# Kernel tuning notes

Hardware: AMD Instinct MI355X
Metric: run time of the kernel (lower is better)

Reference implementation:

```python
import jax, jax.numpy as jnp
import numpy as np


def setup_inputs() -> dict:
    key = jax.random.key(0)
    kq, kk, kv = jax.random.split(key, 3)
    B, T, D = 32, 2048, 64
    return {
        "queries": jax.random.normal(kq, (B, T, D), dtype=jnp.float32),
        "keys": jax.random.normal(kk, (B, T, D), dtype=jnp.float32),
        "values": jax.random.normal(kv, (B, T, D), dtype=jnp.float32),
    }


def reference(queries, keys, values):
    # scores: [B, T, T] = Q K^T / sqrt(d)
    d = queries.shape[-1]
    scale = 1.0 / jnp.sqrt(jnp.asarray(d, dtype=queries.dtype))
    scores = jnp.einsum("btd,bsd->bts", queries, keys) * scale
    T = scores.shape[-1]
    # causal lower-triangular mask; masked positions -> -inf before softmax
    causal = jnp.tril(jnp.ones((T, T), dtype=bool))
    scores = jnp.where(causal[None, :, :], scores, -jnp.inf)
    attn = jax.nn.softmax(scores, axis=-1)
    # eval mode: no dropout
    return jnp.einsum("bts,bsd->btd", attn, values)
```

## Files before the change

### kernel.cpp

```cpp
#include <hip/hip_runtime.h>
#include <hip/hip_bf16.h>

typedef __bf16 bf16;
typedef bf16 bf16x2 __attribute__((ext_vector_type(2)));
typedef bf16 bf16x8 __attribute__((ext_vector_type(8)));
typedef float f32x2 __attribute__((ext_vector_type(2)));
typedef float f32x4 __attribute__((ext_vector_type(4)));
typedef float f32x16 __attribute__((ext_vector_type(16)));
typedef unsigned int uint;

namespace {
constexpr int kB  = 32;
constexpr int kT  = 2048;
constexpr int kD  = 64;
constexpr int QB  = 128;
constexpr int KVB = 64;
constexpr float THR = 8.f;
}

__global__ __launch_bounds__(256, 2)
void fa_fwd(const float* __restrict__ Qg, const float* __restrict__ Kg,
            const float* __restrict__ Vg, float* __restrict__ Og) {
  const int tid  = (int)threadIdx.x;
  const int wid  = tid >> 6;
  const int lane = tid & 63;
  const int hi   = lane >> 5;
  const int ql   = lane & 31;

  const int bid = (int)blockIdx.x;
  const int b   = bid & (kB - 1);
  const int qb  = (kT / QB - 1) - (bid >> 5);
  const int q0  = qb * QB;
  const int qw  = q0 + wid * 32;
  const int qrow = qw + ql;

  __shared__ __align__(16) char smem[4 * 32 * 36 * 4];
  bf16* lK = (bf16*)smem;
  bf16* lV = (bf16*)(smem + 8192);

  const float* Qb = Qg + ((size_t)b * kT + qw) * kD;
  const float* Kb = Kg + (size_t)b * kT * kD;
  const float* Vb = Vg + (size_t)b * kT * kD;
  float*       Ob = Og + ((size_t)b * kT + qw) * kD;

  bf16x8 qf[4];
#pragma unroll
  for (int db = 0; db < 4; ++db) {
    const float* s = Qb + (size_t)ql * kD + db * 16 + hi * 8;
    f32x4 f0 = *(const f32x4*)s, f1 = *(const f32x4*)(s + 4);
    bf16x8 q;
#pragma unroll
    for (int j = 0; j < 4; ++j) {
      q[j]     = (bf16)(f0[j] * 0.125f);
      q[j + 4] = (bf16)(f1[j] * 0.125f);
    }
    qf[db] = q;
  }

  f32x16 ot0 = {}, ot1 = {};
  float m_s = -1e30f, l_s = 0.f;

  const int krow = tid >> 2;
  const int kc16 = (tid & 3) << 4;
  const int vkey = (tid & 31) << 1;
  const int vd0  = (tid >> 5) << 3;

  f32x4 kp0, kp1, kp2, kp3, vp0, vp1, vp2, vp3;

#define LOADK(KV)                                                      \
  {                                                                    \
    const float* s_ = Kb + (size_t)((KV) + krow) * kD + kc16;          \
    kp0 = ((const f32x4*)s_)[0]; kp1 = ((const f32x4*)s_)[1];          \
    kp2 = ((const f32x4*)s_)[2]; kp3 = ((const f32x4*)s_)[3];          \
  }
#define LOADV(KV)                                                      \
  {                                                                    \
    const float* s0_ = Vb + (size_t)((KV) + vkey) * kD + vd0;          \
    const float* s1_ = s0_ + kD;                                       \
    vp0 = ((const f32x4*)s0_)[0]; vp1 = ((const f32x4*)s0_)[1];        \
    vp2 = ((const f32x4*)s1_)[0]; vp3 = ((const f32x4*)s1_)[1];        \
  }
#define STAGEK()                                                       \
  {                                                                    \
    bf16x8 h0_, h1_;                                                   \
    _Pragma("unroll") for (int j = 0; j < 4; ++j) {                    \
      h0_[j] = (bf16)kp0[j]; h0_[j + 4] = (bf16)kp1[j];                \
      h1_[j] = (bf16)kp2[j]; h1_[j + 4] = (bf16)kp3[j];                \
    }                                                                  \
    *(bf16x8*)&lK[(krow * 64 + kc16)     ^ ((krow & 7) << 3)] = h0_;   \
    *(bf16x8*)&lK[(krow * 64 + kc16 + 8) ^ ((krow & 7) << 3)] = h1_;   \
  }
#define STAGEV()                                                       \
  {                                                                    \
    _Pragma("unroll") for (int j = 0; j < 8; ++j) {                    \
      int d_ = vd0 + j;                                                \
      float a0_ = (j < 4) ? vp0[j] : vp1[j - 4];                       \
      float a1_ = (j < 4) ? vp2[j] : vp3[j - 4];                       \
      int e_ = (d_ * 64 + vkey) ^ ((d_ & 7) << 3);                     \
      *(bf16x2*)&lV[e_] = (bf16x2){(bf16)a0_, (bf16)a1_};              \
    }                                                                  \
  }

  LOADK(0) LOADV(0)
  const int kv_end = q0 + QB;
  for (int kv = 0; kv < kv_end; kv += KVB) {
    STAGEK() STAGEV()
    __syncthreads();
    if (kv + KVB < kv_end) { LOADK(kv + KVB) LOADV(kv + KVB) }

    if (kv <= qw) {
      const int nkb = (kv + 32 <= qw) ? 2 : 1;

      f32x16 st0 = {}, st1 = {};
      __builtin_amdgcn_s_setprio(1);
#pragma unroll
      for (int db = 0; db < 4; ++db) {
        bf16x8 kf = *(const bf16x8*)&lK[(ql * 64 + db * 16 + hi * 8) ^ ((ql & 7) << 3)];
        st0 = __builtin_amdgcn_mfma_f32_32x32x16_bf16(kf, qf[db], st0, 0, 0, 0);
      }
      if (nkb == 2) {
        const int r1 = 32 + ql;
#pragma unroll
        for (int db = 0; db < 4; ++db) {
          bf16x8 kf = *(const bf16x8*)&lK[(r1 * 64 + db * 16 + hi * 8) ^ ((r1 & 7) << 3)];
          st1 = __builtin_amdgcn_mfma_f32_32x32x16_bf16(kf, qf[db], st1, 0, 0, 0);
        }
      }
      __builtin_amdgcn_s_setprio(0);

      if (kv + (nkb << 5) > qw) {
#pragma unroll
        for (int reg = 0; reg < 16; ++reg) {
          int krel = (reg & 3) + 8 * (reg >> 2) + 4 * hi;
          if (kv + krel > qrow) st0[reg] = -1e30f;
          if (nkb == 2 && kv + 32 + krel > qrow) st1[reg] = -1e30f;
        }
      }

      float mx = -1e30f;
#pragma unroll
      for (int r = 0; r < 16; ++r) mx = fmaxf(mx, st0[r]);
      if (nkb == 2) {
#pragma unroll
        for (int r = 0; r < 16; ++r) mx = fmaxf(mx, st1[r]);
      }
      mx = fmaxf(mx, __shfl_xor(mx, 32));
      const bool defer = (__all((mx - m_s) <= THR) != 0);
      float mn = m_s;
      if (!defer) {
        mn = fmaxf(m_s, mx);
        float corr = __expf(m_s - mn);
        m_s = mn;
        l_s *= corr;
#pragma unroll
        for (int r = 0; r < 16; ++r) { ot0[r] *= corr; ot1[r] *= corr; }
      }
      float ls = 0.f;
#pragma unroll
      for (int r = 0; r < 16; ++r) { float p = __expf(st0[r] - mn); st0[r] = p; ls += p; }
      if (nkb == 2) {
#pragma unroll
        for (int r = 0; r < 16; ++r) { float p = __expf(st1[r] - mn); st1[r] = p; ls += p; }
      }
      ls += __shfl_xor(ls, 32);
      l_s += ls;

      uint w_[16];
#pragma unroll
      for (int m = 0; m < 8; ++m) {
        bf16x2 t = {(bf16)st0[2 * m], (bf16)st0[2 * m + 1]};
        w_[m] = __builtin_bit_cast(uint, t);
      }
      if (nkb == 2) {
#pragma unroll
        for (int m = 0; m < 8; ++m) {
          bf16x2 t = {(bf16)st1[2 * m], (bf16)st1[2 * m + 1]};
          w_[8 + m] = __builtin_bit_cast(uint, t);
        }
      }

#pragma unroll
      for (int ks = 0; ks < 4; ++ks) {
        if (ks < 2 * nkb) {
          const int mb = (ks >> 1) * 8 + (ks & 1) * 4;
          uint a0 = w_[mb], a1 = w_[mb + 1], b0 = w_[mb + 2], b1 = w_[mb + 3];
          asm volatile("v_permlane32_swap_b32 %0, %1" : "+v"(a0), "+v"(b0));
          asm volatile("v_permlane32_swap_b32 %0, %1" : "+v"(a1), "+v"(b1));
          union { uint u[4]; bf16x8 v; } pc;
          pc.u[0] = a0; pc.u[1] = a1; pc.u[2] = b0; pc.u[3] = b1;
          const bf16x8 pf = pc.v;
          __builtin_amdgcn_s_setprio(1);
          {
            bf16x8 vf0 = *(const bf16x8*)&lV[(ql * 64 + ks * 16 + hi * 8) ^ ((ql & 7) << 3)];
            ot0 = __builtin_amdgcn_mfma_f32_32x32x16_bf16(vf0, pf, ot0, 0, 0, 0);
            const int d1 = 32 + ql;
            bf16x8 vf1 = *(const bf16x8*)&lV[(d1 * 64 + ks * 16 + hi * 8) ^ ((d1 & 7) << 3)];
            ot1 = __builtin_amdgcn_mfma_f32_32x32x16_bf16(vf1, pf, ot1, 0, 0, 0);
          }
          __builtin_amdgcn_s_setprio(0);
        }
      }
    }
    __syncthreads();
  }

  const float inv = 1.0f / l_s;
  float* ep = (float*)(void*)smem + wid * (32 * 36);
#pragma unroll
  for (int dt = 0; dt < 2; ++dt) {
    __syncthreads();
#pragma unroll
    for (int m = 0; m < 8; ++m) {
      int d = ((2 * m) & 3) + 8 * (m >> 1) + 4 * hi;
      f32x2 v;
      v[0] = (dt ? ot1[2 * m]     : ot0[2 * m])     * inv;
      v[1] = (dt ? ot1[2 * m + 1] : ot0[2 * m + 1]) * inv;
      *(f32x2*)&ep[ql * 36 + d] = v;
    }
    __syncthreads();
#pragma unroll
    for (int p = 0; p < 4; ++p) {
      int q = p * 8 + (lane >> 3);
      int c = (lane & 7) * 4;
      f32x4 v = *(const f32x4*)&ep[q * 36 + c];
      *(f32x4*)&Ob[(size_t)q * kD + dt * 32 + c] = v;
    }
  }
}

extern "C" void kernel_launch(void* const* d_in, const int* in_sizes, int n_in,
                              void* d_out, int out_size, void* d_ws, size_t ws_size,
                              hipStream_t stream) {
  const float* Q = (const float*)d_in[0];
  const float* K = (const float*)d_in[1];
  const float* V = (const float*)d_in[2];
  float* O = (float*)d_out;
  dim3 grid(kB * (kT / QB));
  fa_fwd<<<grid, 256, 0, stream>>>(Q, K, V, O);
}
```

Baseline: 129.1 us.

## Split long causal query blocks across two KV halves with merge kernel

Query blocks 8-15, which have the longest causal KV ranges, are each split into two work items covering halves of the KV range. The partial unnormalized outputs plus row max and sum go to a workspace, and a second kernel merges them with log-sum-exp weights. The aim is to balance per-block work and cut the tail from long blocks. The cost is workspace traffic and an extra kernel launch. It only runs when the workspace is large enough.

```diff
diff --git a/kernel.cpp b/kernel.cpp
--- a/kernel.cpp
+++ b/kernel.cpp
@@ -14,13 +14,15 @@
 constexpr int kT  = 2048;
 constexpr int kD  = 64;
 constexpr int QB  = 128;
-constexpr int KVB = 64;
 constexpr float THR = 8.f;
+constexpr int CHUNK_F = 128 * 64 + 128 + 128;
+constexpr size_t WS_NEED = (size_t)512 * CHUNK_F * 4;
 }
 
 __global__ __launch_bounds__(256, 2)
-void fa_fwd(const float* __restrict__ Qg, const float* __restrict__ Kg,
-            const float* __restrict__ Vg, float* __restrict__ Og) {
+void fa_part(const float* __restrict__ Qg, const float* __restrict__ Kg,
+             const float* __restrict__ Vg, float* __restrict__ Og,
+             float* __restrict__ Wg, int mode) {
   const int tid  = (int)threadIdx.x;
   const int wid  = tid >> 6;
   const int lane = tid & 63;
@@ -28,10 +30,20 @@
   const int ql   = lane & 31;
 
   const int bid = (int)blockIdx.x;
-  const int b   = bid & (kB - 1);
-  const int qb  = (kT / QB - 1) - (bid >> 5);
-  const int q0  = qb * QB;
-  const int qw  = q0 + wid * 32;
+  const int b   = bid & 31;
+  const int u   = bid >> 5;
+  int j, t0, t1, sc = 0; bool split;
+  if (mode) {
+    static const signed char JT[24] = {15,15,7,14,14,13,13,6,12,12,11,11,5,10,10,9,9,4,8,8,3,2,1,0};
+    static const signed char HT[24] = { 0, 1,-1, 0, 1, 0, 1,-1, 0, 1, 0, 1,-1, 0, 1, 0, 1,-1, 0, 1,-1,-1,-1,-1};
+    j = JT[u]; const int h = HT[u];
+    if (h < 0) { split = false; t0 = 0; t1 = 2 * (j + 1); }
+    else { split = true; t0 = h * (j + 1); t1 = t0 + (j + 1); sc = b * 16 + 2 * (15 - j) + h; }
+  } else {
+    j = 15 - u; split = false; t0 = 0; t1 = 2 * (j + 1);
+  }
+  const int q0   = j * QB;
+  const int qw   = q0 + wid * 32;
   const int qrow = qw + ql;
 
   __shared__ __align__(16) char smem[4 * 32 * 36 * 4];
@@ -50,9 +62,9 @@
     f32x4 f0 = *(const f32x4*)s, f1 = *(const f32x4*)(s + 4);
     bf16x8 q;
 #pragma unroll
-    for (int j = 0; j < 4; ++j) {
-      q[j]     = (bf16)(f0[j] * 0.125f);
-      q[j + 4] = (bf16)(f1[j] * 0.125f);
+    for (int jj = 0; jj < 4; ++jj) {
+      q[jj]     = (bf16)(f0[jj] * 0.125f);
+      q[jj + 4] = (bf16)(f1[jj] * 0.125f);
     }
     qf[db] = q;
   }
@@ -83,30 +95,30 @@
 #define STAGEK()                                                       \
   {                                                                    \
     bf16x8 h0_, h1_;                                                   \
-    _Pragma("unroll") for (int j = 0; j < 4; ++j) {                    \
-      h0_[j] = (bf16)kp0[j]; h0_[j + 4] = (bf16)kp1[j];                \
-      h1_[j] = (bf16)kp2[j]; h1_[j + 4] = (bf16)kp3[j];                \
+    _Pragma("unroll") for (int jj = 0; jj < 4; ++jj) {                 \
+      h0_[jj] = (bf16)kp0[jj]; h0_[jj + 4] = (bf16)kp1[jj];            \
+      h1_[jj] = (bf16)kp2[jj]; h1_[jj + 4] = (bf16)kp3[jj];            \
     }                                                                  \
     *(bf16x8*)&lK[(krow * 64 + kc16)     ^ ((krow & 7) << 3)] = h0_;   \
     *(bf16x8*)&lK[(krow * 64 + kc16 + 8) ^ ((krow & 7) << 3)] = h1_;   \
   }
 #define STAGEV()                                                       \
   {                                                                    \
-    _Pragma("unroll") for (int j = 0; j < 8; ++j) {                    \
-      int d_ = vd0 + j;                                                \
-      float a0_ = (j < 4) ? vp0[j] : vp1[j - 4];                       \
-      float a1_ = (j < 4) ? vp2[j] : vp3[j - 4];                       \
+    _Pragma("unroll") for (int jj = 0; jj < 8; ++jj) {                 \
+      int d_ = vd0 + jj;                                               \
+      float a0_ = (jj < 4) ? vp0[jj] : vp1[jj - 4];                    \
+      float a1_ = (jj < 4) ? vp2[jj] : vp3[jj - 4];                    \
       int e_ = (d_ * 64 + vkey) ^ ((d_ & 7) << 3);                     \
       *(bf16x2*)&lV[e_] = (bf16x2){(bf16)a0_, (bf16)a1_};              \
     }                                                                  \
   }
 
-  LOADK(0) LOADV(0)
-  const int kv_end = q0 + QB;
-  for (int kv = 0; kv < kv_end; kv += KVB) {
+  const int kv0 = t0 * 64, kv1 = t1 * 64;
+  LOADK(kv0) LOADV(kv0)
+  for (int kv = kv0; kv < kv1; kv += 64) {
     STAGEK() STAGEV()
     __syncthreads();
-    if (kv + KVB < kv_end) { LOADK(kv + KVB) LOADV(kv + KVB) }
+    if (kv + 64 < kv1) { LOADK(kv + 64) LOADV(kv + 64) }
 
     if (kv <= qw) {
       const int nkb = (kv + 32 <= qw) ? 2 : 1;
@@ -186,8 +198,8 @@
           uint a0 = w_[mb], a1 = w_[mb + 1], b0 = w_[mb + 2], b1 = w_[mb + 3];
           asm volatile("v_permlane32_swap_b32 %0, %1" : "+v"(a0), "+v"(b0));
           asm volatile("v_permlane32_swap_b32 %0, %1" : "+v"(a1), "+v"(b1));
-          union { uint u[4]; bf16x8 v; } pc;
-          pc.u[0] = a0; pc.u[1] = a1; pc.u[2] = b0; pc.u[3] = b1;
+          union { uint u4[4]; bf16x8 v; } pc;
+          pc.u4[0] = a0; pc.u4[1] = a1; pc.u4[2] = b0; pc.u4[3] = b1;
           const bf16x8 pf = pc.v;
           __builtin_amdgcn_s_setprio(1);
           {
@@ -204,7 +216,8 @@
     __syncthreads();
   }
 
-  const float inv = 1.0f / l_s;
+  const float scl = split ? 1.0f : (1.0f / l_s);
+  float* outp = split ? (Wg + (size_t)sc * CHUNK_F + (size_t)(wid * 32) * kD) : Ob;
   float* ep = (float*)(void*)smem + wid * (32 * 36);
 #pragma unroll
   for (int dt = 0; dt < 2; ++dt) {
@@ -213,18 +226,51 @@
     for (int m = 0; m < 8; ++m) {
       int d = ((2 * m) & 3) + 8 * (m >> 1) + 4 * hi;
       f32x2 v;
-      v[0] = (dt ? ot1[2 * m]     : ot0[2 * m])     * inv;
-      v[1] = (dt ? ot1[2 * m + 1] : ot0[2 * m + 1]) * inv;
+      v[0] = (dt ? ot1[2 * m]     : ot0[2 * m])     * scl;
+      v[1] = (dt ? ot1[2 * m + 1] : ot0[2 * m + 1]) * scl;
       *(f32x2*)&ep[ql * 36 + d] = v;
     }
     __syncthreads();
 #pragma unroll
     for (int p = 0; p < 4; ++p) {
       int q = p * 8 + (lane >> 3);
-      int c = (lane & 7) * 4;
-      f32x4 v = *(const f32x4*)&ep[q * 36 + c];
-      *(f32x4*)&Ob[(size_t)q * kD + dt * 32 + c] = v;
-    }
+      int cc = (lane & 7) * 4;
+      f32x4 v = *(const f32x4*)&ep[q * 36 + cc];
+      *(f32x4*)&outp[(size_t)q * kD + dt * 32 + cc] = v;
+    }
+  }
+  if (split && hi == 0) {
+    float* wm = Wg + (size_t)sc * CHUNK_F + 8192;
+    wm[wid * 32 + ql]       = m_s;
+    wm[128 + wid * 32 + ql] = l_s;
+  }
+}
+
+__global__ __launch_bounds__(256)
+void fa_merge(const float* __restrict__ Wg, float* __restrict__ Og) {
+  const int bid = (int)blockIdx.x;
+  const int b = bid >> 3, e = bid & 7;
+  const int j = 8 + e;
+  const float* w0 = Wg + (size_t)(b * 16 + 2 * (15 - j)) * CHUNK_F;
+  const float* w1 = w0 + CHUNK_F;
+  const int tid = (int)threadIdx.x;
+  const int r = tid >> 1, ch = (tid & 1) * 32;
+  const float m0 = w0[8192 + r], m1 = w1[8192 + r];
+  const float l0 = w0[8320 + r], l1 = w1[8320 + r];
+  const float M = fmaxf(m0, m1);
+  float a = __expf(m0 - M), c = __expf(m1 - M);
+  const float inv = 1.0f / (a * l0 + c * l1);
+  a *= inv; c *= inv;
+  float* orow = Og + ((size_t)b * kT + (size_t)j * QB + r) * kD + ch;
+  const float* p0 = w0 + (size_t)r * kD + ch;
+  const float* p1 = w1 + (size_t)r * kD + ch;
+#pragma unroll
+  for (int k = 0; k < 8; ++k) {
+    f32x4 x0 = ((const f32x4*)p0)[k], x1 = ((const f32x4*)p1)[k];
+    f32x4 o;
+#pragma unroll
+    for (int q = 0; q < 4; ++q) o[q] = a * x0[q] + c * x1[q];
+    ((f32x4*)orow)[k] = o;
   }
 }
 
@@ -235,6 +281,8 @@
   const float* K = (const float*)d_in[1];
   const float* V = (const float*)d_in[2];
   float* O = (float*)d_out;
-  dim3 grid(kB * (kT / QB));
-  fa_fwd<<<grid, 256, 0, stream>>>(Q, K, V, O);
-}
+  const int mode = (ws_size >= WS_NEED) ? 1 : 0;
+  dim3 grid(mode ? 24 * kB : 16 * kB);
+  fa_part<<<grid, 256, 0, stream>>>(Q, K, V, O, (float*)d_ws, mode);
+  if (mode) fa_merge<<<dim3(256), 256, 0, stream>>>((const float*)d_ws, O);
+}
```

New measurement: 130.7 us. About the same (+1.2%).
